# Kernel optimization log

Measured on AMD Instinct MI355X. Metric: run time of the kernel, lower is better.

## Reference

```python
import jax, jax.numpy as jnp
import numpy as np

NP_ = 20000   # paper nodes
NA_ = 20000   # author nodes
E_AP = 400000
E_PP = 400000
D_IN, D_H, HEADS, D_HEAD, D_FF, D_OUT = 128, 256, 8, 32, 2048, 64


def setup_inputs() -> dict:
    key = jax.random.key(0)
    ks = iter(jax.random.split(key, 48))
    def nrm(shape, s=0.1):
        return jax.random.normal(next(ks), shape, jnp.float32) * s
    inp = {
        'feat_paper': nrm((NP_, D_IN), 1.0),
        'feat_author': nrm((NA_, D_IN), 1.0),
        'W_in_p': nrm((D_H, D_IN)), 'b_in_p': nrm((D_H,), 0.05),
        'W_in_a': nrm((D_H, D_IN)), 'b_in_a': nrm((D_H,), 0.05),
        'W_gat_ap': nrm((D_H, D_H)), 'al_ap': nrm((HEADS, D_HEAD)), 'ar_ap': nrm((HEADS, D_HEAD)), 'b_gat_ap': nrm((D_H,), 0.05),
        'W_gat_pp': nrm((D_H, D_H)), 'al_pp': nrm((HEADS, D_HEAD)), 'ar_pp': nrm((HEADS, D_HEAD)), 'b_gat_pp': nrm((D_H,), 0.05),
        'Wqkv_s': nrm((3 * D_H, D_H)), 'bqkv_s': nrm((3 * D_H,), 0.05), 'Wo_s': nrm((D_H, D_H)), 'bo_s': nrm((D_H,), 0.05),
        'Wqkv_c': nrm((3 * D_H, D_H)), 'bqkv_c': nrm((3 * D_H,), 0.05), 'Wo_c': nrm((D_H, D_H)), 'bo_c': nrm((D_H,), 0.05),
        'W_ff1': nrm((D_FF, D_H)), 'b_ff1': nrm((D_FF,), 0.05),
        'W_ff2': nrm((D_H, D_FF)), 'b_ff2': nrm((D_H,), 0.05),
        'ln1_g': jnp.ones((D_H,), jnp.float32), 'ln1_b': jnp.zeros((D_H,), jnp.float32),
        'ln2_g': jnp.ones((D_H,), jnp.float32), 'ln2_b': jnp.zeros((D_H,), jnp.float32),
        'ln3_g': jnp.ones((D_H,), jnp.float32), 'ln3_b': jnp.zeros((D_H,), jnp.float32),
        'W_pred': nrm((D_OUT, 3 * D_H)), 'b_pred': nrm((D_OUT,), 0.05),
        'ap_src': jax.random.randint(next(ks), (E_AP,), 0, NA_),
        'ap_dst': jax.random.randint(next(ks), (E_AP,), 0, NP_),
        'pp_src': jax.random.randint(next(ks), (E_PP,), 0, NP_),
        'pp_dst': jax.random.randint(next(ks), (E_PP,), 0, NP_),
    }
    return inp


def _leaky(x):
    return jnp.where(x > 0, x, 0.2 * x)  # DGL GATConv negative_slope=0.2


def _gat(x, src, dst, W, al, ar, b):
    """DGL GATConv on homogeneous graph with self-loops appended (eval mode)."""
    N = x.shape[0]
    h = (x @ W.T).reshape(N, HEADS, D_HEAD)          # fc has no bias in GATConv
    el = (h * al[None]).sum(-1)                      # (N, H)
    er = (h * ar[None]).sum(-1)                      # (N, H)
    sl = jnp.arange(N, dtype=src.dtype)              # self loops (add_self_loop)
    s = jnp.concatenate([src, sl])
    d = jnp.concatenate([dst, sl])
    e = _leaky(el[s] + er[d])                        # (E+N, H)
    m = jax.ops.segment_max(e, d, num_segments=N)    # edge-softmax per dst
    a = jnp.exp(e - m[d])
    z = jax.ops.segment_sum(a, d, num_segments=N)
    out = jax.ops.segment_sum(a[:, :, None] * h[s], d, num_segments=N)
    out = out / z[:, :, None] + b.reshape(1, HEADS, D_HEAD)
    return out.reshape(N, D_H)                       # flatten(start_dim=1)


def _ln(x, g, b):
    mu = x.mean(-1, keepdims=True)
    v = ((x - mu) ** 2).mean(-1, keepdims=True)
    return (x - mu) / jnp.sqrt(v + 1e-5) * g + b


def _mha(xq, xkv, Wqkv, bqkv, Wo, bo):
    Wq, Wk, Wv = jnp.split(Wqkv, 3, axis=0)
    bq, bk, bv = jnp.split(bqkv, 3)
    B, S, _ = xq.shape
    Sk = xkv.shape[1]
    q = (xq @ Wq.T + bq).reshape(B, S, HEADS, D_HEAD)
    k = (xkv @ Wk.T + bk).reshape(B, Sk, HEADS, D_HEAD)
    v = (xkv @ Wv.T + bv).reshape(B, Sk, HEADS, D_HEAD)
    att = jnp.einsum('bqhd,bkhd->bhqk', q, k) * (D_HEAD ** -0.5)
    a = jax.nn.softmax(att, axis=-1)
    o = jnp.einsum('bhqk,bkhd->bqhd', a, v).reshape(B, S, D_H)
    return o @ Wo.T + bo


def reference(feat_paper, feat_author, W_in_p, b_in_p, W_in_a, b_in_a,
              W_gat_ap, al_ap, ar_ap, b_gat_ap, W_gat_pp, al_pp, ar_pp, b_gat_pp,
              Wqkv_s, bqkv_s, Wo_s, bo_s, Wqkv_c, bqkv_c, Wo_c, bo_c,
              W_ff1, b_ff1, W_ff2, b_ff2, ln1_g, ln1_b, ln2_g, ln2_b, ln3_g, ln3_b,
              W_pred, b_pred, ap_src, ap_dst, pp_src, pp_dst):
    # fc_in per node type
    hp = feat_paper @ W_in_p.T + b_in_p              # (NP, D_H)
    ha = feat_author @ W_in_a.T + b_in_a             # (NA, D_H)
    Na = ha.shape[0]
    # etype 'ap': bipartite author->paper, to_homogeneous orders [author; paper]
    x_ap = jnp.concatenate([ha, hp], axis=0)
    out_ap = _gat(x_ap, ap_src, ap_dst + Na, W_gat_ap, al_ap, ar_ap, b_gat_ap)[Na:]
    # etype 'pp': paper->paper (single node set)
    out_pp = _gat(hp, pp_src, pp_dst, W_gat_pp, al_pp, ar_pp, b_gat_pp)
    # h dict order: 'paper', 'paper-author', 'paper-paper'
    tgt = jnp.stack([hp, out_ap, out_pp], axis=1)    # (NP, 3, D_H)
    # TransformerDecoderLayer (post-norm, relu, eval): memory = tgt
    x = _ln(tgt + _mha(tgt, tgt, Wqkv_s, bqkv_s, Wo_s, bo_s), ln1_g, ln1_b)
    x = _ln(x + _mha(x, tgt, Wqkv_c, bqkv_c, Wo_c, bo_c), ln2_g, ln2_b)
    ff = jax.nn.relu(x @ W_ff1.T + b_ff1) @ W_ff2.T + b_ff2
    z = _ln(x + ff, ln3_g, ln3_b)
    return z.reshape(z.shape[0], -1) @ W_pred.T + b_pred
```

## Files before the change

kernel.cpp:

```cpp
#include <hip/hip_runtime.h>
#include <hip/hip_bf16.h>
#include <cstdint>
#include <cstddef>

#define NP_N 20000
#define NA_N 20000
#define E_AP_N 400000
#define E_PP_N 400000

typedef __attribute__((ext_vector_type(8))) short bf16x8;
typedef __attribute__((ext_vector_type(4))) float f32x4;

__device__ __forceinline__ float b2f(ushort u) { return __uint_as_float(((uint32_t)u) << 16); }
__device__ __forceinline__ ushort f2b(float f) {
    uint32_t x = __float_as_uint(f);
    return (ushort)((x + 0x7fffu + ((x >> 16) & 1u)) >> 16);
}

#define LGKM_BARRIER() do { \
    asm volatile("s_waitcnt lgkmcnt(0)" ::: "memory"); \
    __builtin_amdgcn_s_barrier(); \
    __builtin_amdgcn_sched_barrier(0); \
} while (0)

#define NJOBS 14
struct PackJobs {
    const float* src[NJOBS];
    void* dst[NJOBS];
    int M[NJOBS], K[NJOBS];
    int type[NJOBS];
    int nquad[NJOBS];
    int blk0[NJOBS];
};

__global__ void pack_all_kernel(PackJobs J)
{
    int b = blockIdx.x;
    int j = 0;
    while (j + 1 < NJOBS && b >= J.blk0[j + 1]) ++j;
    int u = (b - J.blk0[j]) * 256 + threadIdx.x;
    if (u >= J.nquad[j]) return;
    int ty = J.type[j];
    const float* src = J.src[j];
    if (ty == 3) {
        float4 v = ((const float4*)src)[u];
        ushort4 o;
        o.x = f2b(v.x); o.y = f2b(v.y); o.z = f2b(v.z); o.w = f2b(v.w);
        ((ushort4*)J.dst[j])[u] = o;
    } else if (ty == 4) {
        int4 z = {0, 0, 0, 0};
        ((int4*)J.dst[j])[u] = z;
    } else if (ty == 0) {
        int M = J.M[j], K = J.K[j];
        int KT = K >> 5;
        int q = u & 1023;
        int jt = u >> 10;
        int t = jt % KT, jj = jt / KT;
        int ks = q >> 8, rem = q & 255;
        int r = rem >> 1;
        int e0 = (rem & 1) * 4;
        int row = jj * 128 + r;
        ushort4 o = {0, 0, 0, 0};
        if (row < M) {
            const float* s = src + (size_t)row * K + t * 32 + ks * 8 + e0;
            o.x = f2b(s[0]); o.y = f2b(s[1]); o.z = f2b(s[2]); o.w = f2b(s[3]);
        }
        ((ushort4*)J.dst[j])[u] = o;
    } else if (ty == 1) {
        int q = u & 2047, chunk = u >> 11;
        int s = q >> 6, rem = q & 63;
        int fl = rem >> 1, e0 = (rem & 1) * 4;
        const float* sp = src + (size_t)(chunk * 32 + fl) * 256 + s * 8 + e0;
        ushort4 o;
        o.x = f2b(sp[0]); o.y = f2b(sp[1]); o.z = f2b(sp[2]); o.w = f2b(sp[3]);
        ((ushort4*)J.dst[j])[u] = o;
    } else {
        int q = u & 2047, chunk = u >> 11;
        int s2 = q >> 9, rem = q & 511;
        int c = rem >> 1, e0 = (rem & 1) * 4;
        const float* sp = src + (size_t)c * 2048 + chunk * 32 + s2 * 8 + e0;
        ushort4 o;
        o.x = f2b(sp[0]); o.y = f2b(sp[1]); o.z = f2b(sp[2]); o.w = f2b(sp[3]);
        ((ushort4*)J.dst[j])[u] = o;
    }
}

template <int OUT_MODE>
__global__ __launch_bounds__(256) void gemm_mfma(
    const ushort* __restrict__ A, const ushort* __restrict__ Bp,
    const float* __restrict__ bias, void* __restrict__ Cv,
    int N, int M, int K, int lda)
{
    __shared__ __align__(16) ushort Ab[2][4][128 * 8];
    __shared__ __align__(16) ushort Bb[2][4][128 * 8];
    const int tid = threadIdx.x;
    const int lane = tid & 63;
    const int w = tid >> 6;
    const int wr = w >> 1, wc = w & 1;
    const int row0 = blockIdx.x * 128;
    const int col0 = blockIdx.y * 128;
    const int KT = K >> 5;
    const ushort* Bbase = Bp + (size_t)blockIdx.y * KT * 4096;
    f32x4 acc[4][4] = {};

    const int rsub = lane >> 2, ksl = lane & 3;
    int arow[2];
#pragma unroll
    for (int j = 0; j < 2; ++j) {
        int r = row0 + w * 32 + j * 16 + rsub;
        arow[j] = (r < N) ? r : (N - 1);
    }

    bf16x8 areg[2];
    auto loadA = [&](int k0) {
#pragma unroll
        for (int j = 0; j < 2; ++j)
            areg[j] = *(const bf16x8*)(A + (size_t)arow[j] * lda + k0 + ksl * 8);
    };
    auto writeA = [&](int buf) {
#pragma unroll
        for (int j = 0; j < 2; ++j)
            *(bf16x8*)&Ab[buf][ksl][(w * 32 + j * 16 + rsub) * 8] = areg[j];
    };
    auto gloadB = [&](int buf, int t) {
#pragma unroll
        for (int i = 0; i < 2; ++i) {
            const ushort* src = Bbase + (size_t)t * 4096 + (w * 2 + i) * 512 + lane * 8;
            ushort* dst = (ushort*)Bb[buf] + (w * 2 + i) * 512;
            __builtin_amdgcn_global_load_lds(
                (const __attribute__((address_space(1))) void*)src,
                (__attribute__((address_space(3))) void*)dst, 16, 0, 0);
        }
    };

    loadA(0);
    gloadB(0, 0);
    writeA(0);
    __syncthreads();

    for (int t = 0; t < KT; ++t) {
        const int cur = t & 1;
        if (t + 1 < KT) { loadA((t + 1) << 5); gloadB(cur ^ 1, t + 1); }

        bf16x8 af[4], bfr[4];
        const int ks = lane >> 4;
        const int rl = lane & 15;
#pragma unroll
        for (int m = 0; m < 4; ++m)
            af[m] = *(const bf16x8*)&Ab[cur][ks][(wr * 64 + m * 16 + rl) * 8];
#pragma unroll
        for (int n = 0; n < 4; ++n)
            bfr[n] = *(const bf16x8*)&Bb[cur][ks][(wc * 64 + n * 16 + rl) * 8];
#pragma unroll
        for (int m = 0; m < 4; ++m)
#pragma unroll
            for (int n = 0; n < 4; ++n)
                acc[m][n] = __builtin_amdgcn_mfma_f32_16x16x32_bf16(af[m], bfr[n], acc[m][n], 0, 0, 0);

        if (t + 1 < KT) writeA(cur ^ 1);
        __syncthreads();
    }

#pragma unroll
    for (int m = 0; m < 4; ++m) {
#pragma unroll
        for (int n = 0; n < 4; ++n) {
            int gc = col0 + wc * 64 + n * 16 + (lane & 15);
            if (gc >= M) continue;
            float bv = bias ? bias[gc] : 0.f;
#pragma unroll
            for (int r = 0; r < 4; ++r) {
                int grow = row0 + wr * 64 + m * 16 + (lane >> 4) * 4 + r;
                if (grow >= N) continue;
                float v = acc[m][n][r] + bv;
                if (OUT_MODE == 2) v = fmaxf(v, 0.f);
                if (OUT_MODE == 1) ((float*)Cv)[(size_t)grow * M + gc] = v;
                else ((ushort*)Cv)[(size_t)grow * M + gc] = f2b(v);
            }
        }
    }
}

static inline void gemm_bf(const ushort* A, const ushort* Bp, const float* bias, void* C,
                           int N, int M, int K, int lda, int mode, hipStream_t s)
{
    dim3 g((N + 127) / 128, (M + 127) / 128);
    if (mode == 0)      gemm_mfma<0><<<g, 256, 0, s>>>(A, Bp, bias, C, N, M, K, lda);
    else if (mode == 1) gemm_mfma<1><<<g, 256, 0, s>>>(A, Bp, bias, C, N, M, K, lda);
    else                gemm_mfma<2><<<g, 256, 0, s>>>(A, Bp, bias, C, N, M, K, lda);
}

__global__ __launch_bounds__(256, 2) void ff_fused_kernel(
    const ushort* __restrict__ X, const ushort* __restrict__ W1p,
    const ushort* __restrict__ W2p, const float* __restrict__ b1,
    const float* __restrict__ b2, ushort* __restrict__ ffout, int N)
{
    __shared__ __align__(16) ushort W1buf[2][8192];
    __shared__ __align__(16) ushort W2buf[2][8192];
    __shared__ __align__(16) ushort Sbuf[2048];
    const int tid = threadIdx.x;
    const int lane = tid & 63;
    const int w = tid >> 6;
    const int wr = w >> 1, wc = w & 1;
    const int row0 = blockIdx.x * 64;
    const int rl = lane & 15;
    const int ks = lane >> 4;

    bf16x8 xf[2][8];
#pragma unroll
    for (int m = 0; m < 2; ++m) {
        int gr = row0 + wr * 32 + m * 16 + rl;
        if (gr > N - 1) gr = N - 1;
        const ushort* xrow = X + (size_t)gr * 256 + ks * 8;
#pragma unroll
        for (int kc = 0; kc < 8; ++kc)
            xf[m][kc] = *(const bf16x8*)(xrow + kc * 32);
    }

    f32x4 oacc[2][8] = {};

    auto stage = [&](int buf, int fc) {
#pragma unroll
        for (int i = 0; i < 8; ++i) {
            int ii = w * 8 + i;
            const ushort* src;
            ushort* dst;
            if (ii < 16) {
                src = W1p + (size_t)fc * 8192 + ii * 512 + lane * 8;
                dst = &W1buf[buf][ii * 512];
            } else {
                src = W2p + (size_t)fc * 8192 + (ii - 16) * 512 + lane * 8;
                dst = &W2buf[buf][(ii - 16) * 512];
            }
            __builtin_amdgcn_global_load_lds(
                (const __attribute__((address_space(1))) void*)src,
                (__attribute__((address_space(3))) void*)dst, 16, 0, 0);
        }
    };

    stage(0, 0);
    __syncthreads();

    for (int fc = 0; fc < 64; ++fc) {
        const int cur = fc & 1;
        if (fc + 1 < 64) stage(cur ^ 1, fc + 1);

        f32x4 sacc[2] = {};
#pragma unroll
        for (int kc = 0; kc < 8; ++kc) {
            bf16x8 w1f = *(const bf16x8*)&W1buf[cur][(kc * 4 + ks) * 256 + (wc * 16 + rl) * 8];
#pragma unroll
            for (int m = 0; m < 2; ++m)
                sacc[m] = __builtin_amdgcn_mfma_f32_16x16x32_bf16(w1f, xf[m][kc], sacc[m], 0, 0, 0);
        }
        {
            const int f0 = fc * 32;
            const int fb = wc * 16 + ks * 4;
            const int sidx = wc * 2 + (ks >> 1);
            const int e0 = (ks & 1) * 4;
#pragma unroll
            for (int m = 0; m < 2; ++m) {
                ushort4 o;
                o.x = f2b(fmaxf(sacc[m][0] + b1[f0 + fb + 0], 0.f));
                o.y = f2b(fmaxf(sacc[m][1] + b1[f0 + fb + 1], 0.f));
                o.z = f2b(fmaxf(sacc[m][2] + b1[f0 + fb + 2], 0.f));
                o.w = f2b(fmaxf(sacc[m][3] + b1[f0 + fb + 3], 0.f));
                *(ushort4*)&Sbuf[(sidx * 64 + wr * 32 + m * 16 + rl) * 8 + e0] = o;
            }
        }
        LGKM_BARRIER();

        {
            bf16x8 sf[2];
#pragma unroll
            for (int m = 0; m < 2; ++m)
                sf[m] = *(const bf16x8*)&Sbuf[(ks * 512 + (wr * 32 + m * 16 + rl) * 8)];
#pragma unroll
            for (int n = 0; n < 8; ++n) {
                bf16x8 w2f = *(const bf16x8*)&W2buf[cur][ks * 2048 + (wc * 128 + n * 16 + rl) * 8];
#pragma unroll
                for (int m = 0; m < 2; ++m)
                    oacc[m][n] = __builtin_amdgcn_mfma_f32_16x16x32_bf16(sf[m], w2f, oacc[m][n], 0, 0, 0);
            }
        }
        __syncthreads();
    }

#pragma unroll
    for (int n = 0; n < 8; ++n) {
        int c = wc * 128 + n * 16 + rl;
        float bv = b2[c];
#pragma unroll
        for (int m = 0; m < 2; ++m) {
            int rbase = row0 + wr * 32 + m * 16 + ks * 4;
#pragma unroll
            for (int r = 0; r < 4; ++r) {
                int gr = rbase + r;
                if (gr < N) ffout[(size_t)gr * 256 + c] = f2b(oacc[m][n][r] + bv);
            }
        }
    }
}

__global__ void copy_col0_kernel(const ushort* __restrict__ src, ushort* __restrict__ tgt, int n)
{
    int i = blockIdx.x * blockDim.x + threadIdx.x;
    if (i >= n) return;
    int p = i >> 6, c = i & 63;
    ((ushort4*)tgt)[(size_t)p * 192 + c] = ((const ushort4*)src)[(size_t)p * 64 + c];
}

__global__ void attn_lr_all_kernel(
    const ushort* __restrict__ h0, const float* __restrict__ al0, const float* __restrict__ ar0,
    float* __restrict__ el0, float* __restrict__ er0,
    const ushort* __restrict__ h1, const float* __restrict__ al1, const float* __restrict__ ar1,
    float* __restrict__ el1, float* __restrict__ er1)
{
    int idx = blockIdx.x * blockDim.x + threadIdx.x;
    if (idx >= 480000) return;
    const ushort* h; const float *a1, *a2; float *el, *er; int i;
    if (idx < 320000) { h = h0; a1 = al0; a2 = ar0; el = el0; er = er0; i = idx; }
    else { h = h1; a1 = al1; a2 = ar1; el = el1; er = er1; i = idx - 320000; }
    int hd = i & 7;
    const ushort* hp = h + (size_t)(i >> 3) * 256 + hd * 32;
    const float* p1 = a1 + hd * 32;
    const float* p2 = a2 + hd * 32;
    float s1 = 0.f, s2 = 0.f;
#pragma unroll
    for (int j = 0; j < 8; ++j) {
        ushort4 t = ((const ushort4*)hp)[j];
        float v0 = b2f(t.x), v1 = b2f(t.y), v2 = b2f(t.z), v3 = b2f(t.w);
        s1 = fmaf(v0, p1[j * 4 + 0], s1); s2 = fmaf(v0, p2[j * 4 + 0], s2);
        s1 = fmaf(v1, p1[j * 4 + 1], s1); s2 = fmaf(v1, p2[j * 4 + 1], s2);
        s1 = fmaf(v2, p1[j * 4 + 2], s1); s2 = fmaf(v2, p2[j * 4 + 2], s2);
        s1 = fmaf(v3, p1[j * 4 + 3], s1); s2 = fmaf(v3, p2[j * 4 + 3], s2);
    }
    el[i] = s1;
    er[i] = s2;
}

__global__ void count2_kernel(const int* __restrict__ d0, int* __restrict__ c0,
                              const int* __restrict__ d1, int* __restrict__ c1, int E)
{
    int e = blockIdx.x * blockDim.x + threadIdx.x;
    if (e < E) atomicAdd(&c0[d0[e]], 1);
    else if (e < 2 * E) atomicAdd(&c1[d1[e - E]], 1);
}

__global__ void exscan2_kernel(int* __restrict__ deg0, int* __restrict__ offs0,
                               int* __restrict__ deg1, int* __restrict__ offs1, int N)
{
    int* deg = blockIdx.x ? deg1 : deg0;
    int* offs = blockIdx.x ? offs1 : offs0;
    __shared__ int sbuf[1024];
    __shared__ int carry;
    int tid = threadIdx.x;
    if (tid == 0) carry = 0;
    __syncthreads();
    for (int base = 0; base < N; base += 1024) {
        int i = base + tid;
        int v = (i < N) ? deg[i] : 0;
        sbuf[tid] = v;
        __syncthreads();
        for (int off = 1; off < 1024; off <<= 1) {
            int t = (tid >= off) ? sbuf[tid - off] : 0;
            __syncthreads();
            sbuf[tid] += t;
            __syncthreads();
        }
        if (i < N) offs[i] = carry + sbuf[tid] - v;
        int chunk_total = sbuf[1023];
        __syncthreads();
        if (tid == 0) carry += chunk_total;
        __syncthreads();
    }
    if (tid == 0) offs[N] = carry;
    __syncthreads();
    for (int i = tid; i < N; i += 1024) deg[i] = 0;
}

__global__ void scatter2_kernel(const int* __restrict__ s0, const int* __restrict__ d0,
                                const int* __restrict__ o0, int* __restrict__ c0, int* __restrict__ l0,
                                const int* __restrict__ s1, const int* __restrict__ d1,
                                const int* __restrict__ o1, int* __restrict__ c1, int* __restrict__ l1,
                                int E)
{
    int e = blockIdx.x * blockDim.x + threadIdx.x;
    if (e < E) {
        int d = d0[e];
        int pos = atomicAdd(&c0[d], 1);
        l0[o0[d] + pos] = s0[e];
    } else if (e < 2 * E) {
        int e1 = e - E;
        int d = d1[e1];
        int pos = atomicAdd(&c1[d], 1);
        l1[o1[d] + pos] = s1[e1];
    }
}

__global__ __launch_bounds__(64) void gat_agg_all_kernel(
    const ushort* __restrict__ ha, const float* __restrict__ ela, const float* __restrict__ era,
    const int* __restrict__ offsa, const int* __restrict__ lista, const float* __restrict__ biasa,
    const ushort* __restrict__ hp, const float* __restrict__ elp, const float* __restrict__ erp,
    const int* __restrict__ offsp, const int* __restrict__ listp, const float* __restrict__ biasp,
    ushort* __restrict__ out)
{
    int bid = blockIdx.x;
    const ushort* h; const float *el, *er, *bias; const int *offs, *elist;
    int p, dn, coloff;
    if (bid < NP_N) {
        h = ha; el = ela; er = era; offs = offsa; elist = lista; bias = biasa;
        p = bid; dn = NA_N + p; coloff = 256;
    } else {
        h = hp; el = elp; er = erp; offs = offsp; elist = listp; bias = biasp;
        p = bid - NP_N; dn = p; coloff = 512;
    }
    int l = threadIdx.x;
    int head = l >> 3;
    float erv = er[(size_t)dn * 8 + head];
    float acc[4] = {0.f, 0.f, 0.f, 0.f};
    float z = 0.f;
    int beg = offs[p], end = offs[p + 1];
    for (int e = beg - 1; e < end; ++e) {
        int s = (e < beg) ? dn : elist[e];
        float x = el[(size_t)s * 8 + head] + erv;
        x = x > 0.f ? x : 0.2f * x;
        float wgt = expf(x);
        z += wgt;
        ushort4 hv = *(const ushort4*)&h[(size_t)s * 256 + l * 4];
        acc[0] = fmaf(wgt, b2f(hv.x), acc[0]);
        acc[1] = fmaf(wgt, b2f(hv.y), acc[1]);
        acc[2] = fmaf(wgt, b2f(hv.z), acc[2]);
        acc[3] = fmaf(wgt, b2f(hv.w), acc[3]);
    }
    float inv = 1.f / z;
    ushort4 o;
    o.x = f2b(acc[0] * inv + bias[l * 4 + 0]);
    o.y = f2b(acc[1] * inv + bias[l * 4 + 1]);
    o.z = f2b(acc[2] * inv + bias[l * 4 + 2]);
    o.w = f2b(acc[3] * inv + bias[l * 4 + 3]);
    *(ushort4*)&out[(size_t)p * 768 + coloff + l * 4] = o;
}

__global__ void mha3_kernel(const ushort* qb, int ldq, int qoff,
                            const ushort* kvb, int ldkv, int koff, int voff,
                            ushort* ob, int ldo, int NPn)
{
    int idx = blockIdx.x * blockDim.x + threadIdx.x;
    if (idx >= NPn * 24) return;
    int h = idx & 7;
    int i = (idx >> 3) % 3;
    int p = idx / 24;
    float qr[32];
    {
        const ushort* q = qb + (size_t)(p * 3 + i) * ldq + qoff + h * 32;
#pragma unroll
        for (int j = 0; j < 8; ++j) {
            ushort4 t = ((const ushort4*)q)[j];
            qr[j * 4 + 0] = b2f(t.x); qr[j * 4 + 1] = b2f(t.y);
            qr[j * 4 + 2] = b2f(t.z); qr[j * 4 + 3] = b2f(t.w);
        }
    }
    float s[3];
#pragma unroll
    for (int j = 0; j < 3; ++j) {
        const ushort* k = kvb + (size_t)(p * 3 + j) * ldkv + koff + h * 32;
        float a = 0.f;
#pragma unroll
        for (int t4 = 0; t4 < 8; ++t4) {
            ushort4 t = ((const ushort4*)k)[t4];
            a = fmaf(qr[t4 * 4 + 0], b2f(t.x), a);
            a = fmaf(qr[t4 * 4 + 1], b2f(t.y), a);
            a = fmaf(qr[t4 * 4 + 2], b2f(t.z), a);
            a = fmaf(qr[t4 * 4 + 3], b2f(t.w), a);
        }
        s[j] = a * 0.17677669529663687f;
    }
    float m = fmaxf(s[0], fmaxf(s[1], s[2]));
    float e0 = expf(s[0] - m), e1 = expf(s[1] - m), e2 = expf(s[2] - m);
    float inv = 1.f / (e0 + e1 + e2);
    float aw[3] = {e0 * inv, e1 * inv, e2 * inv};
    float o[32] = {};
#pragma unroll
    for (int j = 0; j < 3; ++j) {
        const ushort* v = kvb + (size_t)(p * 3 + j) * ldkv + voff + h * 32;
#pragma unroll
        for (int t4 = 0; t4 < 8; ++t4) {
            ushort4 t = ((const ushort4*)v)[t4];
            o[t4 * 4 + 0] = fmaf(aw[j], b2f(t.x), o[t4 * 4 + 0]);
            o[t4 * 4 + 1] = fmaf(aw[j], b2f(t.y), o[t4 * 4 + 1]);
            o[t4 * 4 + 2] = fmaf(aw[j], b2f(t.z), o[t4 * 4 + 2]);
            o[t4 * 4 + 3] = fmaf(aw[j], b2f(t.w), o[t4 * 4 + 3]);
        }
    }
    ushort* op = ob + (size_t)(p * 3 + i) * ldo + h * 32;
#pragma unroll
    for (int t4 = 0; t4 < 8; ++t4) {
        ushort4 t;
        t.x = f2b(o[t4 * 4 + 0]); t.y = f2b(o[t4 * 4 + 1]);
        t.z = f2b(o[t4 * 4 + 2]); t.w = f2b(o[t4 * 4 + 3]);
        ((ushort4*)op)[t4] = t;
    }
}

__global__ __launch_bounds__(256) void add_ln_kernel(
    const ushort* __restrict__ a, const ushort* __restrict__ b,
    const float* __restrict__ g, const float* __restrict__ be,
    ushort* __restrict__ out, int rows)
{
    int row = blockIdx.x * 4 + (threadIdx.x >> 6);
    if (row >= rows) return;
    int l = threadIdx.x & 63;
    ushort4 va = *(const ushort4*)&a[(size_t)row * 256 + l * 4];
    ushort4 vb = *(const ushort4*)&b[(size_t)row * 256 + l * 4];
    float v[4];
    v[0] = b2f(va.x) + b2f(vb.x);
    v[1] = b2f(va.y) + b2f(vb.y);
    v[2] = b2f(va.z) + b2f(vb.z);
    v[3] = b2f(va.w) + b2f(vb.w);
    float s = v[0] + v[1] + v[2] + v[3];
#pragma unroll
    for (int off = 32; off; off >>= 1) s += __shfl_xor(s, off);
    float mean = s * (1.f / 256.f);
    float s2 = 0.f;
#pragma unroll
    for (int j = 0; j < 4; ++j) { float d = v[j] - mean; s2 = fmaf(d, d, s2); }
#pragma unroll
    for (int off = 32; off; off >>= 1) s2 += __shfl_xor(s2, off);
    float rstd = rsqrtf(s2 * (1.f / 256.f) + 1e-5f);
    ushort4 o;
    o.x = f2b((v[0] - mean) * rstd * g[l * 4 + 0] + be[l * 4 + 0]);
    o.y = f2b((v[1] - mean) * rstd * g[l * 4 + 1] + be[l * 4 + 1]);
    o.z = f2b((v[2] - mean) * rstd * g[l * 4 + 2] + be[l * 4 + 2]);
    o.w = f2b((v[3] - mean) * rstd * g[l * 4 + 3] + be[l * 4 + 3]);
    *(ushort4*)&out[(size_t)row * 256 + l * 4] = o;
}

extern "C" void kernel_launch(void* const* d_in, const int* in_sizes, int n_in,
                              void* d_out, int out_size, void* d_ws, size_t ws_size,
                              hipStream_t stream)
{
    const float* feat_paper  = (const float*)d_in[0];
    const float* feat_author = (const float*)d_in[1];
    const float* W_in_p  = (const float*)d_in[2];
    const float* b_in_p  = (const float*)d_in[3];
    const float* W_in_a  = (const float*)d_in[4];
    const float* b_in_a  = (const float*)d_in[5];
    const float* W_gat_ap = (const float*)d_in[6];
    const float* al_ap    = (const float*)d_in[7];
    const float* ar_ap    = (const float*)d_in[8];
    const float* b_gat_ap = (const float*)d_in[9];
    const float* W_gat_pp = (const float*)d_in[10];
    const float* al_pp    = (const float*)d_in[11];
    const float* ar_pp    = (const float*)d_in[12];
    const float* b_gat_pp = (const float*)d_in[13];
    const float* Wqkv_s = (const float*)d_in[14];
    const float* bqkv_s = (const float*)d_in[15];
    const float* Wo_s   = (const float*)d_in[16];
    const float* bo_s   = (const float*)d_in[17];
    const float* Wqkv_c = (const float*)d_in[18];
    const float* bqkv_c = (const float*)d_in[19];
    const float* Wo_c   = (const float*)d_in[20];
    const float* bo_c   = (const float*)d_in[21];
    const float* W_ff1  = (const float*)d_in[22];
    const float* b_ff1  = (const float*)d_in[23];
    const float* W_ff2  = (const float*)d_in[24];
    const float* b_ff2  = (const float*)d_in[25];
    const float* ln1_g  = (const float*)d_in[26];
    const float* ln1_b  = (const float*)d_in[27];
    const float* ln2_g  = (const float*)d_in[28];
    const float* ln2_b  = (const float*)d_in[29];
    const float* ln3_g  = (const float*)d_in[30];
    const float* ln3_b  = (const float*)d_in[31];
    const float* W_pred = (const float*)d_in[32];
    const float* b_pred = (const float*)d_in[33];
    const int* ap_src = (const int*)d_in[34];
    const int* ap_dst = (const int*)d_in[35];
    const int* pp_src = (const int*)d_in[36];
    const int* pp_dst = (const int*)d_in[37];

    const int NP = NP_N, NA = NA_N;

    uint8_t* wsb = (uint8_t*)d_ws;
    ushort* tgt_bf = (ushort*)wsb;
    ushort* X_bf   = (ushort*)(wsb + 30720000);
    ushort* WB     = (ushort*)(wsb + 61440000);
    ushort* p_in_p   = WB + 0;
    ushort* p_in_a   = WB + 32768;
    ushort* p_gat_ap = WB + 65536;
    ushort* p_gat_pp = WB + 131072;
    ushort* p_qkv_s  = WB + 196608;
    ushort* p_o_s    = WB + 393216;
    ushort* p_qkv_c  = WB + 458752;
    ushort* p_o_c    = WB + 655360;
    ushort* p_pred   = WB + 720896;
    ushort* p_ff1    = WB + 819200;
    ushort* p_ff2    = WB + 1343488;
    uint8_t* BIG = wsb + 65280000;

    ushort* feat_p_bf = (ushort*)BIG;
    ushort* feat_a_bf = (ushort*)(BIG + 5120000);
    ushort* x_ap_bf   = (ushort*)(BIG + 10240000);
    ushort* hp_bf     = x_ap_bf + (size_t)NA * 256;
    ushort* h_ap_bf   = (ushort*)(BIG + 30720000);
    ushort* h_pp_bf   = (ushort*)(BIG + 51200000);
    float* el_ap = (float*)(BIG + 61440000);
    float* er_ap = (float*)(BIG + 62720000);
    float* el_pp = (float*)(BIG + 64000000);
    float* er_pp = (float*)(BIG + 64640000);
    int* ireg    = (int*)(BIG + 65280000);
    int* ap_offs = ireg;
    int* pp_offs = ireg + 20004;
    int* ap_cur  = ireg + 40008;
    int* pp_cur  = ireg + 60008;
    int* ap_list = ireg + 80008;
    int* pp_list = ireg + 480008;

    {
        PackJobs J;
        const float* srcs[NJOBS] = { feat_paper, feat_author, W_in_p, W_in_a, W_gat_ap,
                                     W_gat_pp, Wqkv_s, Wo_s, Wqkv_c, Wo_c, W_pred,
                                     W_ff1, W_ff2, nullptr };
        void* dsts[NJOBS] = { feat_p_bf, feat_a_bf, p_in_p, p_in_a, p_gat_ap,
                              p_gat_pp, p_qkv_s, p_o_s, p_qkv_c, p_o_c, p_pred,
                              p_ff1, p_ff2, ap_cur };
        int Ms[NJOBS]  = {0,0, 256,256,256,256, 768,256,768,256, 64, 0,0, 0};
        int Ks[NJOBS]  = {0,0, 128,128,256,256, 256,256,256,256, 768, 0,0, 0};
        int tys[NJOBS] = {3,3, 0,0,0,0, 0,0,0,0, 0, 1,2, 4};
        int nq[NJOBS]  = {640000,640000, 8192,8192,16384,16384, 49152,16384,49152,16384,
                          24576, 131072,131072, 10000};
        int acc = 0;
        for (int j = 0; j < NJOBS; ++j) {
            J.src[j] = srcs[j]; J.dst[j] = dsts[j];
            J.M[j] = Ms[j]; J.K[j] = Ks[j]; J.type[j] = tys[j]; J.nquad[j] = nq[j];
            J.blk0[j] = acc;
            acc += (nq[j] + 255) / 256;
        }
        pack_all_kernel<<<acc, 256, 0, stream>>>(J);
    }

    gemm_bf(feat_a_bf, p_in_a, b_in_a, x_ap_bf, NA, 256, 128, 128, 0, stream);
    gemm_bf(feat_p_bf, p_in_p, b_in_p, hp_bf,   NP, 256, 128, 128, 0, stream);

    copy_col0_kernel<<<(NP * 64 + 255) / 256, 256, 0, stream>>>(hp_bf, tgt_bf, NP * 64);

    gemm_bf(x_ap_bf, p_gat_ap, nullptr, h_ap_bf, NA + NP, 256, 256, 256, 0, stream);
    gemm_bf(hp_bf,   p_gat_pp, nullptr, h_pp_bf, NP,      256, 256, 256, 0, stream);

    attn_lr_all_kernel<<<1875, 256, 0, stream>>>(h_ap_bf, al_ap, ar_ap, el_ap, er_ap,
                                                 h_pp_bf, al_pp, ar_pp, el_pp, er_pp);

    count2_kernel<<<3125, 256, 0, stream>>>(ap_dst, ap_cur, pp_dst, pp_cur, E_AP_N);
    exscan2_kernel<<<2, 1024, 0, stream>>>(ap_cur, ap_offs, pp_cur, pp_offs, NP);
    scatter2_kernel<<<3125, 256, 0, stream>>>(ap_src, ap_dst, ap_offs, ap_cur, ap_list,
                                              pp_src, pp_dst, pp_offs, pp_cur, pp_list, E_AP_N);

    gat_agg_all_kernel<<<2 * NP, 64, 0, stream>>>(
        h_ap_bf, el_ap, er_ap, ap_offs, ap_list, b_gat_ap,
        h_pp_bf, el_pp, er_pp, pp_offs, pp_list, b_gat_pp, tgt_bf);

    {
        ushort* qkv = (ushort*)BIG;
        gemm_bf(tgt_bf, p_qkv_s, bqkv_s, qkv, 60000, 768, 256, 256, 0, stream);
        mha3_kernel<<<(NP * 24 + 255) / 256, 256, 0, stream>>>(qkv, 768, 0, qkv, 768, 256, 512, qkv, 768, NP);
        gemm_bf(qkv, p_o_s, bo_s, X_bf, 60000, 256, 256, 768, 0, stream);
        add_ln_kernel<<<15000, 256, 0, stream>>>(tgt_bf, X_bf, ln1_g, ln1_b, X_bf, 60000);
    }

    {
        ushort* qb  = (ushort*)BIG;
        ushort* kvb = (ushort*)(BIG + 30720000);
        const ushort* p_kv_c = p_qkv_c + (size_t)2 * 8 * 4096;
        gemm_bf(X_bf,   p_qkv_c, bqkv_c,       qb,  60000, 256, 256, 256, 0, stream);
        gemm_bf(tgt_bf, p_kv_c,  bqkv_c + 256, kvb, 60000, 512, 256, 256, 0, stream);
        mha3_kernel<<<(NP * 24 + 255) / 256, 256, 0, stream>>>(qb, 256, 0, kvb, 512, 0, 256, qb, 256, NP);
        gemm_bf(qb, p_o_c, bo_c, kvb, 60000, 256, 256, 256, 0, stream);
        add_ln_kernel<<<15000, 256, 0, stream>>>(X_bf, kvb, ln2_g, ln2_b, X_bf, 60000);
    }

    {
        ushort* ffo = (ushort*)BIG;
        ff_fused_kernel<<<(60000 + 63) / 64, 256, 0, stream>>>(X_bf, p_ff1, p_ff2, b_ff1, b_ff2, ffo, 60000);
        add_ln_kernel<<<15000, 256, 0, stream>>>(X_bf, ffo, ln3_g, ln3_b, X_bf, 60000);
    }

    gemm_bf(X_bf, p_pred, b_pred, (float*)d_out, NP, 64, 768, 768, 1, stream);
}
```

Before: 817.3 us.

## Triple-buffer GEMM with direct LDS loads and widen fused FFN block

The generic MFMA GEMM now loads the A tile straight into LDS with global_load_lds instead of going through registers. It also triple-buffers A and B, using vmcnt-based waits and a single barrier per K step, so loads for step t+2 overlap compute on step t. The fused FFN kernel moves to 512 threads covering 128 rows per block, which halves how often the W1/W2 chunks are streamed per row. It also merges the two per-iteration barriers into one and vectorizes the bias load. The trade-offs are more LDS per GEMM block and fewer resident FFN blocks, which may lower occupancy.

```diff
diff --git a/kernel.cpp b/kernel.cpp
--- a/kernel.cpp
+++ b/kernel.cpp
@@ -91,8 +91,8 @@
     const float* __restrict__ bias, void* __restrict__ Cv,
     int N, int M, int K, int lda)
 {
-    __shared__ __align__(16) ushort Ab[2][4][128 * 8];
-    __shared__ __align__(16) ushort Bb[2][4][128 * 8];
+    __shared__ __align__(16) ushort Ab[3][4096];
+    __shared__ __align__(16) ushort Bb[3][4096];
     const int tid = threadIdx.x;
     const int lane = tid & 63;
     const int w = tid >> 6;
@@ -103,62 +103,60 @@
     const ushort* Bbase = Bp + (size_t)blockIdx.y * KT * 4096;
     f32x4 acc[4][4] = {};
 
-    const int rsub = lane >> 2, ksl = lane & 3;
-    int arow[2];
-#pragma unroll
-    for (int j = 0; j < 2; ++j) {
-        int r = row0 + w * 32 + j * 16 + rsub;
-        arow[j] = (r < N) ? r : (N - 1);
-    }
-
-    bf16x8 areg[2];
-    auto loadA = [&](int k0) {
-#pragma unroll
-        for (int j = 0; j < 2; ++j)
-            areg[j] = *(const bf16x8*)(A + (size_t)arow[j] * lda + k0 + ksl * 8);
+    size_t aoff[2];
+#pragma unroll
+    for (int i = 0; i < 2; ++i) {
+        int r = row0 + i * 64 + lane;
+        if (r > N - 1) r = N - 1;
+        aoff[i] = (size_t)r * lda + w * 8;
+    }
+
+    auto stage = [&](int buf, int t) {
+        const int k0 = t << 5;
+#pragma unroll
+        for (int i = 0; i < 2; ++i) {
+            __builtin_amdgcn_global_load_lds(
+                (const __attribute__((address_space(1))) void*)(A + aoff[i] + k0),
+                (__attribute__((address_space(3))) void*)(&Ab[buf][(w * 2 + i) * 512]), 16, 0, 0);
+        }
+#pragma unroll
+        for (int i = 0; i < 2; ++i) {
+            __builtin_amdgcn_global_load_lds(
+                (const __attribute__((address_space(1))) void*)(Bbase + (size_t)t * 4096 + (w * 2 + i) * 512 + lane * 8),
+                (__attribute__((address_space(3))) void*)(&Bb[buf][(w * 2 + i) * 512]), 16, 0, 0);
+        }
     };
-    auto writeA = [&](int buf) {
-#pragma unroll
-        for (int j = 0; j < 2; ++j)
-            *(bf16x8*)&Ab[buf][ksl][(w * 32 + j * 16 + rsub) * 8] = areg[j];
-    };
-    auto gloadB = [&](int buf, int t) {
-#pragma unroll
-        for (int i = 0; i < 2; ++i) {
-            const ushort* src = Bbase + (size_t)t * 4096 + (w * 2 + i) * 512 + lane * 8;
-            ushort* dst = (ushort*)Bb[buf] + (w * 2 + i) * 512;
-            __builtin_amdgcn_global_load_lds(
-                (const __attribute__((address_space(1))) void*)src,
-                (__attribute__((address_space(3))) void*)dst, 16, 0, 0);
-        }
-    };
-
-    loadA(0);
-    gloadB(0, 0);
-    writeA(0);
-    __syncthreads();
-
+
+    stage(0, 0);
+    stage(1, 1);
+
+    int cur = 0;
     for (int t = 0; t < KT; ++t) {
-        const int cur = t & 1;
-        if (t + 1 < KT) { loadA((t + 1) << 5); gloadB(cur ^ 1, t + 1); }
+        if (t + 1 < KT) { asm volatile("s_waitcnt vmcnt(4)" ::: "memory"); }
+        else            { asm volatile("s_waitcnt vmcnt(0)" ::: "memory"); }
+        __builtin_amdgcn_s_barrier();
+        __builtin_amdgcn_sched_barrier(0);
+        if (t + 2 < KT) {
+            int nb = cur - 1; if (nb < 0) nb = 2;
+            stage(nb, t + 2);
+        }
 
         bf16x8 af[4], bfr[4];
         const int ks = lane >> 4;
         const int rl = lane & 15;
 #pragma unroll
         for (int m = 0; m < 4; ++m)
-            af[m] = *(const bf16x8*)&Ab[cur][ks][(wr * 64 + m * 16 + rl) * 8];
+            af[m] = *(const bf16x8*)&Ab[cur][ks * 1024 + (wr * 64 + m * 16 + rl) * 8];
 #pragma unroll
         for (int n = 0; n < 4; ++n)
-            bfr[n] = *(const bf16x8*)&Bb[cur][ks][(wc * 64 + n * 16 + rl) * 8];
+            bfr[n] = *(const bf16x8*)&Bb[cur][ks * 1024 + (wc * 64 + n * 16 + rl) * 8];
 #pragma unroll
         for (int m = 0; m < 4; ++m)
 #pragma unroll
             for (int n = 0; n < 4; ++n)
                 acc[m][n] = __builtin_amdgcn_mfma_f32_16x16x32_bf16(af[m], bfr[n], acc[m][n], 0, 0, 0);
 
-        if (t + 1 < KT) writeA(cur ^ 1);
-        __syncthreads();
+        cur = (cur == 2) ? 0 : cur + 1;
     }
 
 #pragma unroll
@@ -190,19 +188,19 @@
     else                gemm_mfma<2><<<g, 256, 0, s>>>(A, Bp, bias, C, N, M, K, lda);
 }
 
-__global__ __launch_bounds__(256, 2) void ff_fused_kernel(
+__global__ __launch_bounds__(512) void ff_fused_kernel(
     const ushort* __restrict__ X, const ushort* __restrict__ W1p,
     const ushort* __restrict__ W2p, const float* __restrict__ b1,
     const float* __restrict__ b2, ushort* __restrict__ ffout, int N)
 {
     __shared__ __align__(16) ushort W1buf[2][8192];
     __shared__ __align__(16) ushort W2buf[2][8192];
-    __shared__ __align__(16) ushort Sbuf[2048];
+    __shared__ __align__(16) ushort Sbuf[4096];
     const int tid = threadIdx.x;
     const int lane = tid & 63;
     const int w = tid >> 6;
     const int wr = w >> 1, wc = w & 1;
-    const int row0 = blockIdx.x * 64;
+    const int row0 = blockIdx.x * 128;
     const int rl = lane & 15;
     const int ks = lane >> 4;
 
@@ -221,8 +219,8 @@
 
     auto stage = [&](int buf, int fc) {
 #pragma unroll
-        for (int i = 0; i < 8; ++i) {
-            int ii = w * 8 + i;
+        for (int i = 0; i < 4; ++i) {
+            int ii = w * 4 + i;
             const ushort* src;
             ushort* dst;
             if (ii < 16) {
@@ -239,10 +237,12 @@
     };
 
     stage(0, 0);
-    __syncthreads();
 
     for (int fc = 0; fc < 64; ++fc) {
         const int cur = fc & 1;
+        asm volatile("s_waitcnt vmcnt(0)" ::: "memory");
+        __builtin_amdgcn_s_barrier();
+        __builtin_amdgcn_sched_barrier(0);
         if (fc + 1 < 64) stage(cur ^ 1, fc + 1);
 
         f32x4 sacc[2] = {};
@@ -258,14 +258,15 @@
             const int fb = wc * 16 + ks * 4;
             const int sidx = wc * 2 + (ks >> 1);
             const int e0 = (ks & 1) * 4;
+            float4 b1v = *(const float4*)&b1[f0 + fb];
 #pragma unroll
             for (int m = 0; m < 2; ++m) {
                 ushort4 o;
-                o.x = f2b(fmaxf(sacc[m][0] + b1[f0 + fb + 0], 0.f));
-                o.y = f2b(fmaxf(sacc[m][1] + b1[f0 + fb + 1], 0.f));
-                o.z = f2b(fmaxf(sacc[m][2] + b1[f0 + fb + 2], 0.f));
-                o.w = f2b(fmaxf(sacc[m][3] + b1[f0 + fb + 3], 0.f));
-                *(ushort4*)&Sbuf[(sidx * 64 + wr * 32 + m * 16 + rl) * 8 + e0] = o;
+                o.x = f2b(fmaxf(sacc[m][0] + b1v.x, 0.f));
+                o.y = f2b(fmaxf(sacc[m][1] + b1v.y, 0.f));
+                o.z = f2b(fmaxf(sacc[m][2] + b1v.z, 0.f));
+                o.w = f2b(fmaxf(sacc[m][3] + b1v.w, 0.f));
+                *(ushort4*)&Sbuf[(sidx * 128 + wr * 32 + m * 16 + rl) * 8 + e0] = o;
             }
         }
         LGKM_BARRIER();
@@ -274,7 +275,7 @@
             bf16x8 sf[2];
 #pragma unroll
             for (int m = 0; m < 2; ++m)
-                sf[m] = *(const bf16x8*)&Sbuf[(ks * 512 + (wr * 32 + m * 16 + rl) * 8)];
+                sf[m] = *(const bf16x8*)&Sbuf[(ks * 128 + wr * 32 + m * 16 + rl) * 8];
 #pragma unroll
             for (int n = 0; n < 8; ++n) {
                 bf16x8 w2f = *(const bf16x8*)&W2buf[cur][ks * 2048 + (wc * 128 + n * 16 + rl) * 8];
@@ -283,7 +284,6 @@
                     oacc[m][n] = __builtin_amdgcn_mfma_f32_16x16x32_bf16(sf[m], w2f, oacc[m][n], 0, 0, 0);
             }
         }
-        __syncthreads();
     }
 
 #pragma unroll
@@ -680,7 +680,7 @@
 
     {
         ushort* ffo = (ushort*)BIG;
-        ff_fused_kernel<<<(60000 + 63) / 64, 256, 0, stream>>>(X_bf, p_ff1, p_ff2, b_ff1, b_ff2, ffo, 60000);
+        ff_fused_kernel<<<(60000 + 127) / 128, 512, 0, stream>>>(X_bf, p_ff1, p_ff2, b_ff1, b_ff2, ffo, 60000);
         add_ln_kernel<<<15000, 256, 0, stream>>>(X_bf, ffo, ln3_g, ln3_b, X_bf, 60000);
     }
 
```

Measured after the change: 869.3 us. +6.4%, slower.
